# Kernel optimization log

Hardware: AMD Instinct MI355X
Metric: run time of the kernel (lower is better)

The kernel has to match this reference:

```python
import jax, jax.numpy as jnp
import numpy as np
import math

B, S, D, H = 4, 1024, 1024, 16
HD = D // H
R = 128  # max_rel_pos
EPS = 1e-5

def setup_inputs() -> dict:
    key = jax.random.key(0)
    ks = jax.random.split(key, 20)
    sd = 1.0 / math.sqrt(D)
    def lin(k, din, dout):
        return jax.random.normal(k, (din, dout), jnp.float32) * (1.0 / math.sqrt(din))
    return {
        "x": jax.random.normal(ks[0], (B, S, D), jnp.float32),
        "wq": lin(ks[1], D, D), "bq": jnp.zeros((D,), jnp.float32),
        "wk": lin(ks[2], D, D), "bk": jnp.zeros((D,), jnp.float32),
        "wv": lin(ks[3], D, D), "bv": jnp.zeros((D,), jnp.float32),
        "wo": lin(ks[4], D, D), "bo": jnp.zeros((D,), jnp.float32),
        "rel_embed": jax.random.normal(ks[5], (2 * R + 1, HD), jnp.float32),
        "ln1_g": jnp.ones((D,), jnp.float32), "ln1_b": jnp.zeros((D,), jnp.float32),
        "ln2_g": jnp.ones((D,), jnp.float32), "ln2_b": jnp.zeros((D,), jnp.float32),
        "w1": lin(ks[6], D, 4 * D), "b1": jnp.zeros((4 * D,), jnp.float32),
        "w2": lin(ks[7], 4 * D, D), "b2": jnp.zeros((D,), jnp.float32),
    }

def _layernorm(x, g, b):
    mu = jnp.mean(x, axis=-1, keepdims=True)
    var = jnp.mean(jnp.square(x - mu), axis=-1, keepdims=True)
    return (x - mu) * jax.lax.rsqrt(var + EPS) * g + b

def _block(x, wq, bq, wk, bk, wv, bv, wo, bo, rel_embed,
           ln1_g, ln1_b, ln2_g, ln2_b, w1, b1, w2, b2):
    h = _layernorm(x, ln1_g, ln1_b)
    # project and split heads: [B,S,D] -> [B,H,S,HD]
    def heads(y):
        return y.reshape(B, S, H, HD).transpose(0, 2, 1, 3)
    Q = heads(h @ wq + bq)
    K = heads(h @ wk + bk)
    V = heads(h @ wv + bv)
    scale = 1.0 / math.sqrt(HD)
    scores = jnp.einsum("bhqd,bhkd->bhqk", Q, K) * scale
    # relative positions: clamp(q-k, -R, R) + R
    pos = jnp.arange(S)
    rel_idx = jnp.clip(pos[None, :] - pos[:, None], -R, R) + R  # [S,S]
    rel = rel_embed[rel_idx]  # [S,S,HD]
    scores = scores + jnp.einsum("bhqd,qkd->bhqk", Q, rel) * scale
    attn = jax.nn.softmax(scores, axis=-1)
    out = jnp.einsum("bhqk,bhkd->bhqd", attn, V)
    out = out.transpose(0, 2, 1, 3).reshape(B, S, D) @ wo + bo
    x = x + out  # dropout is identity in eval
    h2 = _layernorm(x, ln2_g, ln2_b)
    ff = jax.nn.gelu(h2 @ w1 + b1, approximate=False) @ w2 + b2
    return x + ff

def reference(x, wq, bq, wk, bk, wv, bv, wo, bo, rel_embed,
              ln1_g, ln1_b, ln2_g, ln2_b, w1, b1, w2, b2):
    return _block(x, wq, bq, wk, bk, wv, bv, wo, bo, rel_embed,
                  ln1_g, ln1_b, ln2_g, ln2_b, w1, b1, w2, b2)
```

## Files before the change

### kernel.cpp

```cpp
#include <hip/hip_runtime.h>

typedef unsigned short u16;
typedef __bf16 bf16x8 __attribute__((ext_vector_type(8)));
typedef float f32x4 __attribute__((ext_vector_type(4)));

#define QSCALE 0.18033688011112042f

__device__ __forceinline__ float b2f(u16 x) {
    unsigned int u = ((unsigned int)x) << 16;
    return __builtin_bit_cast(float, u);
}
__device__ __forceinline__ u16 f2bf(float f) {
    unsigned int u = __builtin_bit_cast(unsigned int, f);
    u += 0x7fffu + ((u >> 16) & 1u);
    return (u16)(u >> 16);
}
__device__ __forceinline__ void lds_load16(const u16* g, u16* l) {
    __builtin_amdgcn_global_load_lds(
        (const __attribute__((address_space(1))) void*)g,
        (__attribute__((address_space(3))) void*)l, 16, 0, 0);
}

__global__ void transpose_f32_bf16(const float* __restrict__ in, u16* __restrict__ out,
                                   int R, int C) {
    __shared__ u16 tile[32][33];
    int bx = blockIdx.x * 32, by = blockIdx.y * 32;
    int tx = threadIdx.x, ty = threadIdx.y;
#pragma unroll
    for (int i = 0; i < 32; i += 8)
        tile[ty + i][tx] = f2bf(in[(size_t)(by + ty + i) * C + bx + tx]);
    __syncthreads();
#pragma unroll
    for (int i = 0; i < 32; i += 8)
        out[(size_t)(bx + ty + i) * R + by + tx] = tile[tx][ty + i];
}

__global__ void transpose_v(const u16* __restrict__ in, int ldin, int coloff,
                            u16* __restrict__ out) {
    __shared__ u16 tile[32][33];
    size_t zout = (size_t)blockIdx.z << 20;
    int bx = blockIdx.x * 32, by = blockIdx.y * 32;
    int tx = threadIdx.x, ty = threadIdx.y;
#pragma unroll
    for (int i = 0; i < 32; i += 8)
        tile[ty + i][tx] =
            in[(size_t)(blockIdx.z * 1024 + by + ty + i) * ldin + coloff + bx + tx];
    __syncthreads();
#pragma unroll
    for (int i = 0; i < 32; i += 8)
        out[zout + (size_t)(bx + ty + i) * 1024 + by + tx] = tile[tx][ty + i];
}

__global__ void cvt_f32_bf16(const float* __restrict__ in, u16* __restrict__ out, int n) {
    int i = blockIdx.x * 256 + threadIdx.x;
    if (i < n) out[i] = f2bf(in[i]);
}

__global__ void fill_f32(float* __restrict__ p, float v, int n) {
    int i = blockIdx.x * 256 + threadIdx.x;
    if (i < n) p[i] = v;
}

__global__ void concat3(const float* a, const float* b, const float* c, float* o) {
    int i = blockIdx.x * 256 + threadIdx.x;
    o[i] = (i < 1024) ? a[i] : (i < 2048 ? b[i - 1024] : c[i - 2048]);
}

__global__ __launch_bounds__(256) void ln_kernel(
    const float* __restrict__ inf, const float* __restrict__ g,
    const float* __restrict__ b, u16* __restrict__ out) {
    int row = blockIdx.x, t = threadIdx.x;
    size_t base = (size_t)row * 1024 + t * 4;
    float4 f = *(const float4*)(inf + base);
    float v[4] = {f.x, f.y, f.z, f.w};
    float s = v[0] + v[1] + v[2] + v[3];
    float q = v[0] * v[0] + v[1] * v[1] + v[2] * v[2] + v[3] * v[3];
#pragma unroll
    for (int m = 1; m < 64; m <<= 1) {
        s += __shfl_xor(s, m);
        q += __shfl_xor(q, m);
    }
    __shared__ float rs[4], rq[4];
    __shared__ float mu_s, rstd_s;
    int w = t >> 6, lane = t & 63;
    if (lane == 0) { rs[w] = s; rq[w] = q; }
    __syncthreads();
    if (t == 0) {
        float S = rs[0] + rs[1] + rs[2] + rs[3];
        float Q2 = rq[0] + rq[1] + rq[2] + rq[3];
        float mu = S * (1.0f / 1024.0f);
        float var = Q2 * (1.0f / 1024.0f) - mu * mu;
        mu_s = mu;
        rstd_s = rsqrtf(var + 1e-5f);
    }
    __syncthreads();
    float mu = mu_s, rstd = rstd_s;
    u16 o[4];
#pragma unroll
    for (int i = 0; i < 4; i++) {
        int col = t * 4 + i;
        o[i] = f2bf((v[i] - mu) * rstd * g[col] + b[col]);
    }
    uint2 pk;
    pk.x = (unsigned)o[0] | ((unsigned)o[1] << 16);
    pk.y = (unsigned)o[2] | ((unsigned)o[3] << 16);
    *(uint2*)(out + base) = pk;
}

template <int BN>
__global__ __launch_bounds__(256) void gemm_bt(
    const u16* __restrict__ A, int lda, long long sAz,
    const u16* __restrict__ Bt, int ldb, long long sBz, int nclamp,
    const float* __restrict__ bias,
    const float* __restrict__ resid_f32,
    u16* __restrict__ outb, float* __restrict__ outf, int ldc, long long sCz,
    int K, float oscale, int gelu) {
    constexpr int NJ = BN / 32;
    constexpr int NUNITS = 8 + BN / 16;
    constexpr int UPW = NUNITS / 4;
    __shared__ __align__(16) u16 As[2][128 * 32];
    __shared__ __align__(16) u16 Bs[2][BN * 32];
    int t = threadIdx.x, w = t >> 6, lane = t & 63;
    int z = blockIdx.z;
    const u16* Ab = A + (size_t)z * sAz;
    const u16* Bb = Bt + (size_t)z * sBz;
    int m0 = blockIdx.y * 128, n0 = blockIdx.x * BN;
    int lo = lane & 15, hi = lane >> 4;
    int wr = w >> 1, wc = w & 1;
    f32x4 acc[4][NJ];
#pragma unroll
    for (int i = 0; i < 4; i++)
#pragma unroll
        for (int j = 0; j < NJ; j++) acc[i][j] = (f32x4){0.f, 0.f, 0.f, 0.f};

    auto stage = [&](int k0, int buf) {
#pragma unroll
        for (int uu = 0; uu < UPW; ++uu) {
            int u = w * UPW + uu;
            if (u < 8) {
                int s = u * 64 + lane;
                int row = s >> 2, c8 = (s & 3) * 8;
                const u16* gp = Ab + (size_t)(m0 + row) * lda + k0 + c8;
                lds_load16(gp, &As[buf][u * 512]);
            } else {
                int s = (u - 8) * 64 + lane;
                int row = s >> 2, c8 = (s & 3) * 8;
                int n = n0 + row;
                if (n >= nclamp) n = nclamp - 1;
                const u16* gp = Bb + (size_t)n * ldb + k0 + c8;
                lds_load16(gp, &Bs[buf][(u - 8) * 512]);
            }
        }
    };

    int nk = K >> 5;
    stage(0, 0);
    for (int kk = 0; kk < nk; ++kk) {
        __syncthreads();
        if (kk + 1 < nk) stage((kk + 1) << 5, (kk + 1) & 1);
        int buf = kk & 1;
        bf16x8 a[4], bb[NJ];
#pragma unroll
        for (int i = 0; i < 4; i++)
            a[i] = *(const bf16x8*)&As[buf][(wr * 64 + i * 16 + lo) * 32 + 8 * hi];
#pragma unroll
        for (int j = 0; j < NJ; j++)
            bb[j] = *(const bf16x8*)&Bs[buf][(wc * (BN / 2) + j * 16 + lo) * 32 + 8 * hi];
#pragma unroll
        for (int i = 0; i < 4; i++)
#pragma unroll
            for (int j = 0; j < NJ; j++)
                acc[i][j] = __builtin_amdgcn_mfma_f32_16x16x32_bf16(a[i], bb[j], acc[i][j], 0, 0, 0);
    }
#pragma unroll
    for (int j = 0; j < NJ; j++) {
        int col = n0 + wc * (BN / 2) + j * 16 + lo;
        float bv = bias ? bias[col] : 0.f;
#pragma unroll
        for (int i = 0; i < 4; i++) {
            int rbase = m0 + wr * 64 + i * 16 + hi * 4;
#pragma unroll
            for (int r = 0; r < 4; r++) {
                float v = fmaf(acc[i][j][r], oscale, bv);
                if (gelu) v = 0.5f * v * (1.f + erff(v * 0.70710678118654752f));
                size_t ridx = (size_t)(rbase + r) * ldc + col;
                if (resid_f32) v += resid_f32[ridx];
                size_t idx = (size_t)z * sCz + ridx;
                if (outf) outf[idx] = v;
                if (outb) outb[idx] = f2bf(v);
            }
        }
    }
}

__global__ __launch_bounds__(256) void attn_kernel(
    const u16* __restrict__ QKV, const u16* __restrict__ Vtg,
    const u16* __restrict__ Qrel, u16* __restrict__ Ob) {
    __shared__ __align__(16) u16 KsL[2][4096];
    __shared__ __align__(16) u16 VsL[2][4096];
    __shared__ __align__(16) u16 Ps[4][16 * 72];
    int t = threadIdx.x, w = t >> 6, lane = t & 63;
    int bid = blockIdx.x;
    int qblk = bid & 15, h = (bid >> 4) & 15, bb = bid >> 8;
    int lo = lane & 15, hi = lane >> 4;
    int q0b = qblk * 64;
    int q0 = q0b + w * 16;

    const u16* qrow = QKV + ((size_t)(bb * 1024 + q0 + lo) * 3072 + h * 64 + hi * 8);
    bf16x8 qf0 = *(const bf16x8*)qrow;
    bf16x8 qf1 = *(const bf16x8*)(qrow + 32);

    const size_t qrel_base = (size_t)h * (4096ull * 384);
    float blo[4], bhi[4];
#pragma unroll
    for (int r = 0; r < 4; r++) {
        size_t row = qrel_base + (size_t)(bb * 1024 + q0 + hi * 4 + r) * 384;
        blo[r] = b2f(Qrel[row]);
        bhi[r] = b2f(Qrel[row + 256]);
    }

    const u16* Kg = QKV + 1024 + ((size_t)(bb * 1024)) * 3072 + h * 64;
    const u16* Vg = Vtg + ((size_t)(bb * 1024 + h * 64)) * 1024;

    auto stage = [&](int k0, int buf) {
#pragma unroll
        for (int half = 0; half < 2; ++half) {
            int s = half * 256 + w * 64 + lane;
            int row = s >> 3, cg = (s & 7) ^ (row & 7);
            lds_load16(Kg + (size_t)(k0 + row) * 3072 + cg * 8,
                       &KsL[buf][(half * 256 + w * 64) * 8]);
            lds_load16(Vg + (size_t)row * 1024 + k0 + cg * 8,
                       &VsL[buf][(half * 256 + w * 64) * 8]);
        }
    };

    f32x4 oacc[4];
#pragma unroll
    for (int j = 0; j < 4; j++) oacc[j] = (f32x4){0.f, 0.f, 0.f, 0.f};
    float l_[4] = {0.f, 0.f, 0.f, 0.f};

    stage(0, 0);
    for (int c = 0; c < 16; ++c) {
        int k0 = c * 64;
        __syncthreads();
        if (c < 15) stage(k0 + 64, (c + 1) & 1);
        const u16* Ksb = KsL[c & 1];
        const u16* Vsb = VsL[c & 1];

        f32x4 sc[4];
#pragma unroll
        for (int kt = 0; kt < 4; kt++) {
            int row = kt * 16 + lo, rx = row & 7;
            bf16x8 kf0 = *(const bf16x8*)&Ksb[(row * 8 + (hi ^ rx)) * 8];
            bf16x8 kf1 = *(const bf16x8*)&Ksb[(row * 8 + ((4 + hi) ^ rx)) * 8];
            f32x4 zz = (f32x4){0.f, 0.f, 0.f, 0.f};
            sc[kt] = __builtin_amdgcn_mfma_f32_16x16x32_bf16(qf0, kf0, zz, 0, 0, 0);
            sc[kt] = __builtin_amdgcn_mfma_f32_16x16x32_bf16(qf1, kf1, sc[kt], 0, 0, 0);
        }
        float bt[4][4];
        if (k0 + 192 <= q0b) {
#pragma unroll
            for (int kt = 0; kt < 4; kt++)
#pragma unroll
                for (int r = 0; r < 4; r++) bt[kt][r] = blo[r];
        } else if (k0 >= q0b + 192) {
#pragma unroll
            for (int kt = 0; kt < 4; kt++)
#pragma unroll
                for (int r = 0; r < 4; r++) bt[kt][r] = bhi[r];
        } else {
#pragma unroll
            for (int kt = 0; kt < 4; kt++)
#pragma unroll
                for (int r = 0; r < 4; r++) {
                    int q = q0 + hi * 4 + r;
                    int k = k0 + kt * 16 + lo;
                    int p = k - q;
                    p = p < -128 ? -128 : (p > 128 ? 128 : p);
                    p += 128;
                    bt[kt][r] = b2f(Qrel[qrel_base + (size_t)(bb * 1024 + q) * 384 + p]);
                }
        }
#pragma unroll
        for (int kt = 0; kt < 4; kt++)
#pragma unroll
            for (int r = 0; r < 4; r++) {
                float s = fmaf(sc[kt][r], QSCALE, bt[kt][r]);
                float p = __builtin_amdgcn_exp2f(s);
                l_[r] += p;
                Ps[w][(hi * 4 + r) * 72 + kt * 16 + lo] =
                    (u16)(__builtin_bit_cast(unsigned int, p) >> 16);
            }
        bf16x8 pf0 = *(const bf16x8*)&Ps[w][lo * 72 + 8 * hi];
        bf16x8 pf1 = *(const bf16x8*)&Ps[w][lo * 72 + 32 + 8 * hi];
#pragma unroll
        for (int j = 0; j < 4; j++) {
            int row = j * 16 + lo, rx = row & 7;
            bf16x8 vf0 = *(const bf16x8*)&Vsb[(row * 8 + (hi ^ rx)) * 8];
            bf16x8 vf1 = *(const bf16x8*)&Vsb[(row * 8 + ((4 + hi) ^ rx)) * 8];
            oacc[j] = __builtin_amdgcn_mfma_f32_16x16x32_bf16(pf0, vf0, oacc[j], 0, 0, 0);
            oacc[j] = __builtin_amdgcn_mfma_f32_16x16x32_bf16(pf1, vf1, oacc[j], 0, 0, 0);
        }
    }
#pragma unroll
    for (int r = 0; r < 4; r++) {
#pragma unroll
        for (int m = 1; m < 16; m <<= 1) l_[r] += __shfl_xor(l_[r], m);
    }
#pragma unroll
    for (int r = 0; r < 4; r++) {
        float inv = 1.f / l_[r];
        int q = q0 + hi * 4 + r;
#pragma unroll
        for (int j = 0; j < 4; j++)
            Ob[(size_t)(bb * 1024 + q) * 1024 + h * 64 + j * 16 + lo] =
                f2bf(oacc[j][r] * inv);
    }
}

extern "C" void kernel_launch(void* const* d_in, const int* in_sizes, int n_in,
                              void* d_out, int out_size, void* d_ws, size_t ws_size,
                              hipStream_t stream) {
    const float* x   = (const float*)d_in[0];
    const float* wq  = (const float*)d_in[1];
    const float* bq  = (const float*)d_in[2];
    const float* wk  = (const float*)d_in[3];
    const float* bk  = (const float*)d_in[4];
    const float* wv  = (const float*)d_in[5];
    const float* bv  = (const float*)d_in[6];
    const float* wo  = (const float*)d_in[7];
    const float* bo  = (const float*)d_in[8];
    const float* rel = (const float*)d_in[9];
    const float* g1  = (const float*)d_in[10];
    const float* be1 = (const float*)d_in[11];
    const float* g2  = (const float*)d_in[12];
    const float* be2 = (const float*)d_in[13];
    const float* w1  = (const float*)d_in[14];
    const float* bf1 = (const float*)d_in[15];
    const float* w2  = (const float*)d_in[16];
    const float* bf2 = (const float*)d_in[17];

    char* ws = (char*)d_ws;
    const size_t MB = 1024ull * 1024ull;
    u16* wqkvT = (u16*)(ws + 0 * MB);
    u16* wqT  = (u16*)(ws + 0 * MB);
    u16* wkT  = (u16*)(ws + 2 * MB);
    u16* wvT  = (u16*)(ws + 4 * MB);
    u16* woT  = (u16*)(ws + 6 * MB);
    u16* w1T  = (u16*)(ws + 8 * MB);
    u16* w2T  = (u16*)(ws + 16 * MB);
    u16* h    = (u16*)(ws + 24 * MB);
    u16* QKV  = (u16*)(ws + 32 * MB);
    u16* Vtg  = (u16*)(ws + 56 * MB);
    u16* qrel = (u16*)(ws + 64 * MB);
    float* x2 = (float*)(ws + 64 * MB);
    u16* att  = (u16*)(ws + 112 * MB);
    u16* relb = (u16*)(ws + 120 * MB);
    float* cbias = (float*)(ws + 120 * MB + 64 * 1024);
    float* bqkv  = (float*)(ws + 120 * MB + 128 * 1024);
    u16* ff1  = (u16*)(ws + 32 * MB);
    u16* h2   = h;

    dim3 tb(32, 8);
    transpose_f32_bf16<<<dim3(32, 32), tb, 0, stream>>>(wq, wqT, 1024, 1024);
    transpose_f32_bf16<<<dim3(32, 32), tb, 0, stream>>>(wk, wkT, 1024, 1024);
    transpose_f32_bf16<<<dim3(32, 32), tb, 0, stream>>>(wv, wvT, 1024, 1024);
    transpose_f32_bf16<<<dim3(32, 32), tb, 0, stream>>>(wo, woT, 1024, 1024);
    transpose_f32_bf16<<<dim3(128, 32), tb, 0, stream>>>(w1, w1T, 1024, 4096);
    transpose_f32_bf16<<<dim3(32, 128), tb, 0, stream>>>(w2, w2T, 4096, 1024);
    cvt_f32_bf16<<<65, 256, 0, stream>>>(rel, relb, 257 * 64);
    fill_f32<<<2, 256, 0, stream>>>(cbias, -16.0f, 384);
    concat3<<<12, 256, 0, stream>>>(bq, bk, bv, bqkv);

    ln_kernel<<<4096, 256, 0, stream>>>(x, g1, be1, h);

    gemm_bt<64><<<dim3(48, 32, 1), 256, 0, stream>>>(h, 1024, 0, wqkvT, 1024, 0, 3072,
        bqkv, nullptr, QKV, nullptr, 3072, 0, 1024, 1.f, 0);
    transpose_v<<<dim3(32, 32, 4), tb, 0, stream>>>(QKV, 3072, 2048, Vtg);

    gemm_bt<64><<<dim3(6, 32, 16), 256, 0, stream>>>(QKV, 3072, 64, relb, 64, 0, 257,
        cbias, nullptr, qrel, nullptr, 384, (long long)4096 * 384,
        64, QSCALE, 0);

    attn_kernel<<<1024, 256, 0, stream>>>(QKV, Vtg, qrel, att);

    gemm_bt<64><<<dim3(16, 32, 1), 256, 0, stream>>>(att, 1024, 0, woT, 1024, 0, 1024,
        bo, x, nullptr, x2, 1024, 0, 1024, 1.f, 0);

    ln_kernel<<<4096, 256, 0, stream>>>(x2, g2, be2, h2);

    gemm_bt<128><<<dim3(32, 32, 1), 256, 0, stream>>>(h2, 1024, 0, w1T, 1024, 0, 4096,
        bf1, nullptr, ff1, nullptr, 4096, 0, 1024, 1.f, 1);
    gemm_bt<64><<<dim3(16, 32, 1), 256, 0, stream>>>(ff1, 4096, 0, w2T, 4096, 0, 1024,
        bf2, x2, nullptr, (float*)d_out, 1024, 0, 4096, 1.f, 0);
}
```

Before: 457.6 us.

## Remap GEMM blocks per XCD and add K=64 swizzled GEMM for narrow outputs

Flattens the GEMM grid to 1D and remaps block IDs so that each of the 8 XCDs (blocks assigned round-robin by block index) processes a contiguous band of M rows. This is meant to improve L2 reuse of A tiles within each XCD. A new gemm_bt64 kernel with a 64-wide K step and XOR-swizzled LDS layout replaces the output and FF2 projections. It halves the number of k-loop iterations and syncs and aims to avoid LDS bank conflicts, at the cost of twice the LDS per block.

```diff
diff --git a/kernel.cpp b/kernel.cpp
--- a/kernel.cpp
+++ b/kernel.cpp
@@ -114,7 +114,7 @@
     const float* __restrict__ bias,
     const float* __restrict__ resid_f32,
     u16* __restrict__ outb, float* __restrict__ outf, int ldc, long long sCz,
-    int K, float oscale, int gelu) {
+    int K, int nx, int ny, float oscale, int gelu) {
     constexpr int NJ = BN / 32;
     constexpr int NUNITS = 8 + BN / 16;
     constexpr int UPW = NUNITS / 4;
@@ -124,7 +124,9 @@
     int z = blockIdx.z;
     const u16* Ab = A + (size_t)z * sAz;
     const u16* Bb = Bt + (size_t)z * sBz;
-    int m0 = blockIdx.y * 128, n0 = blockIdx.x * BN;
+    int bid = blockIdx.x, xcd = bid & 7, ii = bid >> 3;
+    int xx = ii % nx, yy = xcd * (ny >> 3) + ii / nx;
+    int m0 = yy * 128, n0 = xx * BN;
     int lo = lane & 15, hi = lane >> 4;
     int wr = w >> 1, wc = w & 1;
     f32x4 acc[4][NJ];
@@ -188,6 +190,95 @@
                 size_t idx = (size_t)z * sCz + ridx;
                 if (outf) outf[idx] = v;
                 if (outb) outb[idx] = f2bf(v);
+            }
+        }
+    }
+}
+
+__global__ __launch_bounds__(256) void gemm_bt64(
+    const u16* __restrict__ A, int lda,
+    const u16* __restrict__ Bt, int ldb,
+    const float* __restrict__ bias,
+    const float* __restrict__ resid_f32,
+    u16* __restrict__ outb, float* __restrict__ outf, int ldc,
+    int K, int nx, int ny, float oscale, int gelu) {
+    constexpr int AU = 16, BU = 8, UPW = (AU + BU) / 4;
+    __shared__ __align__(16) u16 As[2][128 * 64];
+    __shared__ __align__(16) u16 Bs[2][64 * 64];
+    int t = threadIdx.x, w = t >> 6, lane = t & 63;
+    int bid = blockIdx.x, xcd = bid & 7, ii = bid >> 3;
+    int xx = ii % nx, yy = xcd * (ny >> 3) + ii / nx;
+    int m0 = yy * 128, n0 = xx * 64;
+    int lo = lane & 15, hi = lane >> 4;
+    int wr = w >> 1, wc = w & 1;
+    f32x4 acc[4][2];
+#pragma unroll
+    for (int i = 0; i < 4; i++)
+#pragma unroll
+        for (int j = 0; j < 2; j++) acc[i][j] = (f32x4){0.f, 0.f, 0.f, 0.f};
+
+    auto stage = [&](int k0, int buf) {
+#pragma unroll
+        for (int uu = 0; uu < UPW; ++uu) {
+            int u = w * UPW + uu;
+            if (u < AU) {
+                int s = u * 64 + lane;
+                int row = s >> 3, cg = (lane & 7) ^ (row & 7);
+                lds_load16(A + (size_t)(m0 + row) * lda + k0 + cg * 8,
+                           &As[buf][u * 512]);
+            } else {
+                int u2 = u - AU;
+                int s = u2 * 64 + lane;
+                int row = s >> 3, cg = (lane & 7) ^ (row & 7);
+                lds_load16(Bt + (size_t)(n0 + row) * ldb + k0 + cg * 8,
+                           &Bs[buf][u2 * 512]);
+            }
+        }
+    };
+
+    int nk = K >> 6;
+    stage(0, 0);
+    for (int kk = 0; kk < nk; ++kk) {
+        __syncthreads();
+        if (kk + 1 < nk) stage((kk + 1) << 6, (kk + 1) & 1);
+        int buf = kk & 1;
+#pragma unroll
+        for (int k2 = 0; k2 < 2; ++k2) {
+            bf16x8 a[4], bb[2];
+#pragma unroll
+            for (int i = 0; i < 4; i++) {
+                int row = wr * 64 + i * 16 + lo;
+                int g = (k2 * 4 + hi) ^ (row & 7);
+                a[i] = *(const bf16x8*)&As[buf][row * 64 + g * 8];
+            }
+#pragma unroll
+            for (int j = 0; j < 2; j++) {
+                int row = wc * 32 + j * 16 + lo;
+                int g = (k2 * 4 + hi) ^ (row & 7);
+                bb[j] = *(const bf16x8*)&Bs[buf][row * 64 + g * 8];
+            }
+#pragma unroll
+            for (int i = 0; i < 4; i++)
+#pragma unroll
+                for (int j = 0; j < 2; j++)
+                    acc[i][j] = __builtin_amdgcn_mfma_f32_16x16x32_bf16(a[i], bb[j], acc[i][j], 0, 0, 0);
+        }
+    }
+#pragma unroll
+    for (int j = 0; j < 2; j++) {
+        int col = n0 + wc * 32 + j * 16 + lo;
+        float bv = bias ? bias[col] : 0.f;
+#pragma unroll
+        for (int i = 0; i < 4; i++) {
+            int rbase = m0 + wr * 64 + i * 16 + hi * 4;
+#pragma unroll
+            for (int r = 0; r < 4; r++) {
+                float v = fmaf(acc[i][j][r], oscale, bv);
+                if (gelu) v = 0.5f * v * (1.f + erff(v * 0.70710678118654752f));
+                size_t ridx = (size_t)(rbase + r) * ldc + col;
+                if (resid_f32) v += resid_f32[ridx];
+                if (outf) outf[ridx] = v;
+                if (outb) outb[ridx] = f2bf(v);
             }
         }
     }
@@ -374,23 +465,23 @@
 
     ln_kernel<<<4096, 256, 0, stream>>>(x, g1, be1, h);
 
-    gemm_bt<64><<<dim3(48, 32, 1), 256, 0, stream>>>(h, 1024, 0, wqkvT, 1024, 0, 3072,
-        bqkv, nullptr, QKV, nullptr, 3072, 0, 1024, 1.f, 0);
+    gemm_bt<64><<<1536, 256, 0, stream>>>(h, 1024, 0, wqkvT, 1024, 0, 3072,
+        bqkv, nullptr, QKV, nullptr, 3072, 0, 1024, 48, 32, 1.f, 0);
     transpose_v<<<dim3(32, 32, 4), tb, 0, stream>>>(QKV, 3072, 2048, Vtg);
 
-    gemm_bt<64><<<dim3(6, 32, 16), 256, 0, stream>>>(QKV, 3072, 64, relb, 64, 0, 257,
+    gemm_bt<64><<<dim3(192, 1, 16), 256, 0, stream>>>(QKV, 3072, 64, relb, 64, 0, 257,
         cbias, nullptr, qrel, nullptr, 384, (long long)4096 * 384,
-        64, QSCALE, 0);
+        64, 6, 32, QSCALE, 0);
 
     attn_kernel<<<1024, 256, 0, stream>>>(QKV, Vtg, qrel, att);
 
-    gemm_bt<64><<<dim3(16, 32, 1), 256, 0, stream>>>(att, 1024, 0, woT, 1024, 0, 1024,
-        bo, x, nullptr, x2, 1024, 0, 1024, 1.f, 0);
+    gemm_bt64<<<512, 256, 0, stream>>>(att, 1024, woT, 1024,
+        bo, x, nullptr, x2, 1024, 1024, 16, 32, 1.f, 0);
 
     ln_kernel<<<4096, 256, 0, stream>>>(x2, g2, be2, h2);
 
-    gemm_bt<128><<<dim3(32, 32, 1), 256, 0, stream>>>(h2, 1024, 0, w1T, 1024, 0, 4096,
-        bf1, nullptr, ff1, nullptr, 4096, 0, 1024, 1.f, 1);
-    gemm_bt<64><<<dim3(16, 32, 1), 256, 0, stream>>>(ff1, 4096, 0, w2T, 4096, 0, 1024,
-        bf2, x2, nullptr, (float*)d_out, 1024, 0, 4096, 1.f, 0);
-}
+    gemm_bt<128><<<1024, 256, 0, stream>>>(h2, 1024, 0, w1T, 1024, 0, 4096,
+        bf1, nullptr, ff1, nullptr, 4096, 0, 1024, 32, 32, 1.f, 1);
+    gemm_bt64<<<512, 256, 0, stream>>>(ff1, 4096, w2T, 4096,
+        bf2, x2, nullptr, (float*)d_out, 1024, 4096, 16, 32, 1.f, 0);
+}
```

New measurement: 473.2 us. 1.03x slower.
